# Optimization experiments

Hardware: AMD Instinct MI355X
Metric: run time of the kernel (lower is better)

## Reference

```python
import jax, jax.numpy as jnp
import numpy as np

N = 768       # num nodes
E = 12288     # num edges (avg degree 16)
D_IN = 6
H = 256       # hidden_dim
TEMPERATURE = 1.0


def gcn_conv(x, W, b, src, dst, n):
    """PyG GCNConv: add self-loops, symmetric deg^-1/2 normalization, then xW aggregation + bias."""
    h = x @ W  # [n, H]
    loop = jnp.arange(n, dtype=src.dtype)
    s = jnp.concatenate([src, loop])
    d = jnp.concatenate([dst, loop])
    deg = jax.ops.segment_sum(jnp.ones(s.shape, dtype=h.dtype), d, num_segments=n)
    dinv = jnp.where(deg > 0, jax.lax.rsqrt(deg), 0.0)
    norm = dinv[s] * dinv[d]  # [E+n]
    out = jax.ops.segment_sum(h[s] * norm[:, None], d, num_segments=n)
    return out + b


def setup_inputs() -> dict:
    key = jax.random.key(0)
    ks = jax.random.split(key, 10)
    sc = lambda fan: np.float32(1.0 / np.sqrt(fan))
    x = jax.random.normal(ks[0], (N, D_IN), jnp.float32)
    edge_index = jax.random.randint(ks[1], (2, E), 0, N, dtype=jnp.int32)
    Wc1 = jax.random.normal(ks[2], (D_IN, H), jnp.float32) * sc(D_IN)
    bc1 = jnp.zeros((H,), jnp.float32)
    Wc2 = jax.random.normal(ks[3], (H, H), jnp.float32) * sc(H)
    bc2 = jnp.zeros((H,), jnp.float32)
    We1 = jax.random.normal(ks[4], (2 * H, H), jnp.float32) * sc(2 * H)
    be1 = jax.random.normal(ks[5], (H,), jnp.float32) * sc(2 * H)
    We2 = jax.random.normal(ks[6], (H, 1), jnp.float32) * sc(H)
    be2 = jax.random.normal(ks[7], (1,), jnp.float32) * sc(H)
    return {"x": x, "edge_index": edge_index, "Wc1": Wc1, "bc1": bc1,
            "Wc2": Wc2, "bc2": bc2, "We1": We1, "be1": be1, "We2": We2, "be2": be2}


def reference(x, edge_index, Wc1, bc1, Wc2, bc2, We1, be1, We2, be2):
    src, dst = edge_index[0], edge_index[1]
    h = jax.nn.elu(gcn_conv(x, Wc1, bc1, src, dst, N))
    h = gcn_conv(h, Wc2, bc2, src, dst, N)  # [N, H]
    # edge scorer: Linear(cat([x_i, x_j])) == x_i @ We1[:H] + x_j @ We1[H:] + be1
    ai = h @ We1[:H]   # [N, H], contribution of x_i (row node)
    aj = h @ We1[H:]   # [N, H], contribution of x_j (col node)
    pair = jax.nn.relu(ai[:, None, :] + aj[None, :, :] + be1)  # [N, N, H]
    logits = jnp.einsum('ijh,h->ij', pair, We2[:, 0]) + be2[0]  # [N, N]
    logits = logits / TEMPERATURE
    logits = jnp.where(jnp.eye(N, dtype=bool), -jnp.inf, logits)
    return jax.nn.softmax(logits, axis=-1)
```

## Files before the change

### kernel.cpp

```cpp
#include <hip/hip_runtime.h>
#include <math.h>

#define N_NODES 768
#define N_EDGES 12288
#define D_INF 6
#define H 256
#define CAP 128
#define SA 260

__global__ __launch_bounds__(768) void k_zero(int* __restrict__ cnt) {
    cnt[threadIdx.x] = 0;
}

__global__ void k_scatter(const int* __restrict__ src, const int* __restrict__ dst,
                          int* __restrict__ cnt, int* __restrict__ slots) {
    int e = blockIdx.x * blockDim.x + threadIdx.x;
    if (e >= N_EDGES) return;
    int d = dst[e];
    int p = atomicAdd(&cnt[d], 1);
    if (p < CAP) slots[d * CAP + p] = src[e];
}

__global__ __launch_bounds__(256) void k_layer1(
    const float* __restrict__ x, const float* __restrict__ Wc1,
    const float* __restrict__ bc1, const int* __restrict__ cnt,
    const int* __restrict__ slots, float* __restrict__ h1) {
    __shared__ int   s_s[CAP];
    __shared__ float s_w[CAP];
    __shared__ float s6[D_INF];
    const int v = blockIdx.x, t = threadIdx.x;
    const int c = cnt[v];
    const int cc = min(c, CAP);
    const float dv = rsqrtf((float)(c + 1));

    if (t < D_INF) s6[t] = dv * dv * x[v * D_INF + t];
    for (int i = t; i < cc; i += 256) {
        int s = slots[v * CAP + i];
        s_s[i] = s;
        s_w[i] = rsqrtf((float)(cnt[s] + 1)) * dv;
    }
    __syncthreads();
    for (int i = t; i < D_INF * cc; i += 256) {
        int n = i / D_INF, k = i - n * D_INF;
        atomicAdd(&s6[k], s_w[n] * x[s_s[n] * D_INF + k]);
    }
    __syncthreads();
    float acc = bc1[t];
    #pragma unroll
    for (int k = 0; k < D_INF; ++k) acc = fmaf(s6[k], Wc1[k * H + t], acc);
    h1[v * H + t] = (acc > 0.f) ? acc : expm1f(acc);
}

__global__ __launch_bounds__(256) void k_agg(
    const float* __restrict__ h1, const int* __restrict__ cnt,
    const int* __restrict__ slots, float* __restrict__ agg2) {
    __shared__ int   s_s[CAP];
    __shared__ float s_w[CAP];
    const int v = blockIdx.x, t = threadIdx.x;
    const int c = cnt[v];
    const int cc = min(c, CAP);
    const float dv = rsqrtf((float)(c + 1));

    for (int i = t; i < cc; i += 256) {
        int s = slots[v * CAP + i];
        s_s[i] = s;
        s_w[i] = rsqrtf((float)(cnt[s] + 1)) * dv;
    }
    __syncthreads();
    float acc = dv * dv * h1[v * H + t];
    #pragma unroll 4
    for (int n = 0; n < cc; ++n)
        acc = fmaf(s_w[n], h1[s_s[n] * H + t], acc);
    agg2[v * H + t] = acc;
}

__global__ __launch_bounds__(256) void k_h2(
    const float* __restrict__ agg2, const float* __restrict__ Wc2,
    const float* __restrict__ bc2, float* __restrict__ h2) {
    __shared__ __align__(16) float s_a[48 * SA];
    __shared__ __align__(16) float s_wT[16 * SA];
    const int t = threadIdx.x, b = blockIdx.x;
    const int rg = b >> 4, cp = b & 15;
    const int j0 = rg * 48, c0 = cp * 16;
    const int c = t & 15, ro = t >> 4;

    for (int i = t; i < 48 * 64; i += 256) {
        int r = i >> 6, q = i & 63;
        float4 v = *(const float4*)(agg2 + (size_t)(j0 + r) * H + q * 4);
        *(float4*)&s_a[r * SA + q * 4] = v;
    }
    {
        int kk = t >> 4, cc = t & 15;
        #pragma unroll
        for (int it = 0; it < 16; ++it) {
            int k = kk + it * 16;
            s_wT[cc * SA + k] = Wc2[(size_t)k * H + c0 + cc];
        }
    }
    __syncthreads();

    float a0 = 0.f, a1 = 0.f, a2 = 0.f;
    #pragma unroll 8
    for (int kg = 0; kg < 64; ++kg) {
        float4 w  = *(const float4*)&s_wT[c * SA + kg * 4];
        float4 v0 = *(const float4*)&s_a[(ro)      * SA + kg * 4];
        float4 v1 = *(const float4*)&s_a[(ro + 16) * SA + kg * 4];
        float4 v2 = *(const float4*)&s_a[(ro + 32) * SA + kg * 4];
        a0 = fmaf(v0.x, w.x, a0); a0 = fmaf(v0.y, w.y, a0);
        a0 = fmaf(v0.z, w.z, a0); a0 = fmaf(v0.w, w.w, a0);
        a1 = fmaf(v1.x, w.x, a1); a1 = fmaf(v1.y, w.y, a1);
        a1 = fmaf(v1.z, w.z, a1); a1 = fmaf(v1.w, w.w, a1);
        a2 = fmaf(v2.x, w.x, a2); a2 = fmaf(v2.y, w.y, a2);
        a2 = fmaf(v2.z, w.z, a2); a2 = fmaf(v2.w, w.w, a2);
    }
    float bb = bc2[c0 + c];
    h2[(size_t)(j0 + ro)      * H + c0 + c] = a0 + bb;
    h2[(size_t)(j0 + ro + 16) * H + c0 + c] = a1 + bb;
    h2[(size_t)(j0 + ro + 32) * H + c0 + c] = a2 + bb;
}

__global__ __launch_bounds__(256) void k_ae(
    const float* __restrict__ h2, const float* __restrict__ We1,
    const float* __restrict__ be1, float* __restrict__ aib,
    float* __restrict__ ajcT) {
    __shared__ __align__(16) float s_h[32 * SA];
    __shared__ __align__(16) float s_waT[16 * SA];
    __shared__ __align__(16) float s_wbT[16 * SA];
    const int t = threadIdx.x, b = blockIdx.x;
    const int rg = b >> 4, cp = b & 15;
    const int j0 = rg * 32, c0 = cp * 16;
    const int c = t & 15, ro = t >> 4;

    for (int i = t; i < 32 * 64; i += 256) {
        int r = i >> 6, q = i & 63;
        float4 v = *(const float4*)(h2 + (size_t)(j0 + r) * H + q * 4);
        *(float4*)&s_h[r * SA + q * 4] = v;
    }
    {
        int kk = t >> 4, cc = t & 15;
        #pragma unroll
        for (int it = 0; it < 16; ++it) {
            int k = kk + it * 16;
            s_waT[cc * SA + k] = We1[(size_t)k * H + c0 + cc];
            s_wbT[cc * SA + k] = We1[(size_t)(H + k) * H + c0 + cc];
        }
    }
    __syncthreads();

    float pa0 = 0.f, pa1 = 0.f, pb0 = 0.f, pb1 = 0.f;
    #pragma unroll 8
    for (int kg = 0; kg < 64; ++kg) {
        float4 wa = *(const float4*)&s_waT[c * SA + kg * 4];
        float4 wb = *(const float4*)&s_wbT[c * SA + kg * 4];
        float4 v0 = *(const float4*)&s_h[(ro)      * SA + kg * 4];
        float4 v1 = *(const float4*)&s_h[(ro + 16) * SA + kg * 4];
        pa0 = fmaf(v0.x, wa.x, pa0); pa0 = fmaf(v0.y, wa.y, pa0);
        pa0 = fmaf(v0.z, wa.z, pa0); pa0 = fmaf(v0.w, wa.w, pa0);
        pa1 = fmaf(v1.x, wa.x, pa1); pa1 = fmaf(v1.y, wa.y, pa1);
        pa1 = fmaf(v1.z, wa.z, pa1); pa1 = fmaf(v1.w, wa.w, pa1);
        pb0 = fmaf(v0.x, wb.x, pb0); pb0 = fmaf(v0.y, wb.y, pb0);
        pb0 = fmaf(v0.z, wb.z, pb0); pb0 = fmaf(v0.w, wb.w, pb0);
        pb1 = fmaf(v1.x, wb.x, pb1); pb1 = fmaf(v1.y, wb.y, pb1);
        pb1 = fmaf(v1.z, wb.z, pb1); pb1 = fmaf(v1.w, wb.w, pb1);
    }
    aib[(size_t)(j0 + ro)      * H + c0 + c] = pa0;
    aib[(size_t)(j0 + ro + 16) * H + c0 + c] = pa1;
    float be = be1[c0 + c];
    ajcT[(size_t)(c0 + c) * N_NODES + j0 + ro]      = pb0 + be;
    ajcT[(size_t)(c0 + c) * N_NODES + j0 + ro + 16] = pb1 + be;
}

__global__ __launch_bounds__(1024) void k_pair(
    const float* __restrict__ aib, const float* __restrict__ ajcT,
    const float* __restrict__ We2, float* __restrict__ out) {
    __shared__ float s_ai[3 * H];
    __shared__ float s_w2[H];
    __shared__ float s_acc[3 * 9 * 256];
    __shared__ float red[3 * 256];
    const int t = threadIdx.x, b = blockIdx.x;
    const int tc = t & 255, th = t >> 8;
    const int i0 = b * 3;

    if (th == 0) s_w2[tc] = We2[tc];
    else s_ai[(th - 1) * H + tc] = aib[(i0 + th - 1) * H + tc];
    __syncthreads();

    float acc[3][3];
    #pragma unroll
    for (int i = 0; i < 3; ++i)
        #pragma unroll
        for (int jj = 0; jj < 3; ++jj) acc[i][jj] = 0.f;

    const int hb = th * 64;
    #pragma unroll 8
    for (int hh = 0; hh < 64; ++hh) {
        int h = hb + hh;
        float wv = s_w2[h];
        float a0v = s_ai[h], a1v = s_ai[256 + h], a2v = s_ai[512 + h];
        const float* col = ajcT + (size_t)h * N_NODES;
        float b0 = col[tc], b1 = col[tc + 256], b2 = col[tc + 512];
        acc[0][0] = fmaf(fmaxf(a0v + b0, 0.f), wv, acc[0][0]);
        acc[0][1] = fmaf(fmaxf(a0v + b1, 0.f), wv, acc[0][1]);
        acc[0][2] = fmaf(fmaxf(a0v + b2, 0.f), wv, acc[0][2]);
        acc[1][0] = fmaf(fmaxf(a1v + b0, 0.f), wv, acc[1][0]);
        acc[1][1] = fmaf(fmaxf(a1v + b1, 0.f), wv, acc[1][1]);
        acc[1][2] = fmaf(fmaxf(a1v + b2, 0.f), wv, acc[1][2]);
        acc[2][0] = fmaf(fmaxf(a2v + b0, 0.f), wv, acc[2][0]);
        acc[2][1] = fmaf(fmaxf(a2v + b1, 0.f), wv, acc[2][1]);
        acc[2][2] = fmaf(fmaxf(a2v + b2, 0.f), wv, acc[2][2]);
    }

    if (th > 0) {
        #pragma unroll
        for (int i = 0; i < 3; ++i)
            #pragma unroll
            for (int jj = 0; jj < 3; ++jj)
                s_acc[((th - 1) * 9 + i * 3 + jj) * 256 + tc] = acc[i][jj];
    }
    __syncthreads();
    if (th == 0) {
        #pragma unroll
        for (int qq = 0; qq < 3; ++qq)
            #pragma unroll
            for (int i = 0; i < 3; ++i)
                #pragma unroll
                for (int jj = 0; jj < 3; ++jj)
                    acc[i][jj] += s_acc[(qq * 9 + i * 3 + jj) * 256 + tc];
        #pragma unroll
        for (int i = 0; i < 3; ++i)
            #pragma unroll
            for (int jj = 0; jj < 3; ++jj)
                if (tc + jj * 256 == i0 + i) acc[i][jj] = -INFINITY;
        #pragma unroll
        for (int i = 0; i < 3; ++i)
            red[i * 256 + tc] = fmaxf(fmaxf(acc[i][0], acc[i][1]), acc[i][2]);
    }
    __syncthreads();
    for (int s = 128; s > 0; s >>= 1) {
        if (t < s) {
            red[t] = fmaxf(red[t], red[t + s]);
            red[256 + t] = fmaxf(red[256 + t], red[256 + t + s]);
            red[512 + t] = fmaxf(red[512 + t], red[512 + t + s]);
        }
        __syncthreads();
    }
    float mx0 = red[0], mx1 = red[256], mx2 = red[512];
    __syncthreads();

    float e[3][3];
    if (th == 0) {
        float s0 = 0.f, s1 = 0.f, s2 = 0.f;
        #pragma unroll
        for (int jj = 0; jj < 3; ++jj) {
            e[0][jj] = __expf(acc[0][jj] - mx0); s0 += e[0][jj];
            e[1][jj] = __expf(acc[1][jj] - mx1); s1 += e[1][jj];
            e[2][jj] = __expf(acc[2][jj] - mx2); s2 += e[2][jj];
        }
        red[tc] = s0; red[256 + tc] = s1; red[512 + tc] = s2;
    }
    __syncthreads();
    for (int s = 128; s > 0; s >>= 1) {
        if (t < s) {
            red[t] += red[t + s];
            red[256 + t] += red[256 + t + s];
            red[512 + t] += red[512 + t + s];
        }
        __syncthreads();
    }
    if (th == 0) {
        float r0 = 1.0f / red[0], r1 = 1.0f / red[256], r2 = 1.0f / red[512];
        #pragma unroll
        for (int jj = 0; jj < 3; ++jj) {
            out[(size_t)(i0 + 0) * N_NODES + tc + jj * 256] = e[0][jj] * r0;
            out[(size_t)(i0 + 1) * N_NODES + tc + jj * 256] = e[1][jj] * r1;
            out[(size_t)(i0 + 2) * N_NODES + tc + jj * 256] = e[2][jj] * r2;
        }
    }
}

extern "C" void kernel_launch(void* const* d_in, const int* in_sizes, int n_in,
                              void* d_out, int out_size, void* d_ws, size_t ws_size,
                              hipStream_t stream) {
    const float* x   = (const float*)d_in[0];
    const int*   ei  = (const int*)d_in[1];
    const float* Wc1 = (const float*)d_in[2];
    const float* bc1 = (const float*)d_in[3];
    const float* Wc2 = (const float*)d_in[4];
    const float* bc2 = (const float*)d_in[5];
    const float* We1 = (const float*)d_in[6];
    const float* be1 = (const float*)d_in[7];
    const float* We2 = (const float*)d_in[8];
    float* out = (float*)d_out;

    char* ws = (char*)d_ws;
    int*   cnt   = (int*)(ws + 0);
    int*   slots = (int*)(ws + 4096);
    float* h1    = (float*)(ws + 397312);
    float* agg2  = (float*)(ws + 1183744);
    float* ajcT  = (float*)(ws + 1970176);
    float* h2    = h1;
    float* aib   = agg2;

    const int* srcA = ei;
    const int* dstA = ei + N_EDGES;

    k_zero<<<1, 768, 0, stream>>>(cnt);
    k_scatter<<<N_EDGES / 256, 256, 0, stream>>>(srcA, dstA, cnt, slots);
    k_layer1<<<N_NODES, 256, 0, stream>>>(x, Wc1, bc1, cnt, slots, h1);
    k_agg<<<N_NODES, 256, 0, stream>>>(h1, cnt, slots, agg2);
    k_h2<<<256, 256, 0, stream>>>(agg2, Wc2, bc2, h2);
    k_ae<<<384, 256, 0, stream>>>(h2, We1, be1, aib, ajcT);
    k_pair<<<N_NODES / 3, 1024, 0, stream>>>(aib, ajcT, We2, out);
}
```

Measured before the change: 58.62 us.

## Fuse graph front-end, precompose Wc2·We1, split pair scoring from softmax

Replaces the zero/scatter/layer1 kernels with one front kernel in which each block redundantly counts degrees over all edges in shared memory and builds its own nodes' neighbor lists. The same launch also precomputes Wc2·[We1a|We1b] and the folded bias, so one GEMM replaces the h2 and edge-embedding GEMMs. The pair-scoring kernel is re-tiled to 12 rows by a quarter of the hidden dim, writing partial logits to workspace, and a separate softmax kernel sums the partials. This cuts launch count and GEMM work, but every front block rescans all edges and the partial logits add extra global traffic.

```diff
diff --git a/kernel.cpp b/kernel.cpp
--- a/kernel.cpp
+++ b/kernel.cpp
@@ -5,50 +5,120 @@
 #define N_EDGES 12288
 #define D_INF 6
 #define H 256
+#define H2 512
 #define CAP 128
+#define LC 256
 #define SA 260
 
-__global__ __launch_bounds__(768) void k_zero(int* __restrict__ cnt) {
-    cnt[threadIdx.x] = 0;
-}
-
-__global__ void k_scatter(const int* __restrict__ src, const int* __restrict__ dst,
-                          int* __restrict__ cnt, int* __restrict__ slots) {
-    int e = blockIdx.x * blockDim.x + threadIdx.x;
-    if (e >= N_EDGES) return;
-    int d = dst[e];
-    int p = atomicAdd(&cnt[d], 1);
-    if (p < CAP) slots[d * CAP + p] = src[e];
-}
-
-__global__ __launch_bounds__(256) void k_layer1(
-    const float* __restrict__ x, const float* __restrict__ Wc1,
-    const float* __restrict__ bc1, const int* __restrict__ cnt,
-    const int* __restrict__ slots, float* __restrict__ h1) {
-    __shared__ int   s_s[CAP];
-    __shared__ float s_w[CAP];
-    __shared__ float s6[D_INF];
-    const int v = blockIdx.x, t = threadIdx.x;
-    const int c = cnt[v];
-    const int cc = min(c, CAP);
-    const float dv = rsqrtf((float)(c + 1));
-
-    if (t < D_INF) s6[t] = dv * dv * x[v * D_INF + t];
-    for (int i = t; i < cc; i += 256) {
-        int s = slots[v * CAP + i];
-        s_s[i] = s;
-        s_w[i] = rsqrtf((float)(cnt[s] + 1)) * dv;
-    }
-    __syncthreads();
-    for (int i = t; i < D_INF * cc; i += 256) {
-        int n = i / D_INF, k = i - n * D_INF;
-        atomicAdd(&s6[k], s_w[n] * x[s_s[n] * D_INF + k]);
-    }
-    __syncthreads();
-    float acc = bc1[t];
-    #pragma unroll
-    for (int k = 0; k < D_INF; ++k) acc = fmaf(s6[k], Wc1[k * H + t], acc);
-    h1[v * H + t] = (acc > 0.f) ? acc : expm1f(acc);
+__global__ __launch_bounds__(256) void k_front(
+    const float* __restrict__ x, const int* __restrict__ ei,
+    const float* __restrict__ Wc1, const float* __restrict__ bc1,
+    const float* __restrict__ Wc2, const float* __restrict__ bc2,
+    const float* __restrict__ We1, const float* __restrict__ be1,
+    int* __restrict__ cnt_g, int* __restrict__ slots,
+    float* __restrict__ h1, float* __restrict__ Wcombo, float* __restrict__ bias_c)
+{
+    const int t = threadIdx.x;
+    if (blockIdx.x < 256) {
+        __shared__ int s_cnt[N_NODES];
+        __shared__ int s_list[LC];
+        __shared__ int s_nm;
+        __shared__ int s_pos[3];
+        __shared__ float s_agg[3][D_INF];
+        const int b = blockIdx.x, v0 = b * 3;
+        const int* src = ei;
+        const int* dst = ei + N_EDGES;
+        for (int v = t; v < N_NODES; v += 256) s_cnt[v] = 0;
+        if (t == 0) s_nm = 0;
+        if (t < 3) s_pos[t] = 0;
+        if (t < 3 * D_INF) ((float*)s_agg)[t] = 0.f;
+        __syncthreads();
+        for (int e = t; e < N_EDGES; e += 256) {
+            int d = dst[e];
+            atomicAdd(&s_cnt[d], 1);
+            unsigned li = (unsigned)(d - v0);
+            if (li < 3u) {
+                int s = src[e];
+                int p = atomicAdd(&s_nm, 1);
+                if (p < LC) s_list[p] = (s << 2) | (int)li;
+            }
+        }
+        __syncthreads();
+        const int nm = min(s_nm, LC);
+        if (t < 3) cnt_g[v0 + t] = s_cnt[v0 + t];
+        for (int m = t; m < nm; m += 256) {
+            int pk = s_list[m];
+            int s = pk >> 2, li = pk & 3;
+            int p = atomicAdd(&s_pos[li], 1);
+            if (p < CAP) slots[(v0 + li) * CAP + p] = s;
+            float w = rsqrtf((float)(s_cnt[s] + 1)) * rsqrtf((float)(s_cnt[v0 + li] + 1));
+            #pragma unroll
+            for (int k = 0; k < D_INF; ++k)
+                atomicAdd(&s_agg[li][k], w * x[s * D_INF + k]);
+        }
+        if (t < 3) {
+            int v = v0 + t;
+            float dv2 = 1.0f / (float)(s_cnt[v] + 1);
+            #pragma unroll
+            for (int k = 0; k < D_INF; ++k)
+                atomicAdd(&s_agg[t][k], dv2 * x[v * D_INF + k]);
+        }
+        __syncthreads();
+        #pragma unroll
+        for (int r = 0; r < 3; ++r) {
+            float acc = bc1[t];
+            #pragma unroll
+            for (int k = 0; k < D_INF; ++k)
+                acc = fmaf(s_agg[r][k], Wc1[k * H + t], acc);
+            h1[(v0 + r) * H + t] = (acc > 0.f) ? acc : expm1f(acc);
+        }
+    } else {
+        __shared__ __align__(16) float s_a[32 * SA];
+        __shared__ __align__(16) float s_bT[16 * SA];
+        __shared__ float s_bc2[H];
+        const int idx = blockIdx.x - 256;
+        const int rg = idx >> 5, cp = idx & 31;
+        const int r0 = rg * 32, c0 = cp * 16;
+        const int c = t & 15, ro = t >> 4;
+        for (int i = t; i < 32 * 64; i += 256) {
+            int r = i >> 6, q = i & 63;
+            float4 v = *(const float4*)(Wc2 + (size_t)(r0 + r) * H + q * 4);
+            *(float4*)&s_a[r * SA + q * 4] = v;
+        }
+        {
+            int kk = t >> 4, cc = t & 15;
+            int cg = c0 + cc;
+            const float* Wsrc = (cg < H) ? (We1 + cg)
+                                         : (We1 + (size_t)H * H + (cg - H));
+            #pragma unroll
+            for (int it = 0; it < 16; ++it) {
+                int k = kk + it * 16;
+                s_bT[cc * SA + k] = Wsrc[(size_t)k * H];
+            }
+        }
+        s_bc2[t] = bc2[t];
+        __syncthreads();
+        float a0 = 0.f, a1 = 0.f;
+        #pragma unroll 8
+        for (int kg = 0; kg < 64; ++kg) {
+            float4 w  = *(const float4*)&s_bT[c * SA + kg * 4];
+            float4 v0 = *(const float4*)&s_a[(ro)      * SA + kg * 4];
+            float4 v1 = *(const float4*)&s_a[(ro + 16) * SA + kg * 4];
+            a0 = fmaf(v0.x, w.x, a0); a0 = fmaf(v0.y, w.y, a0);
+            a0 = fmaf(v0.z, w.z, a0); a0 = fmaf(v0.w, w.w, a0);
+            a1 = fmaf(v1.x, w.x, a1); a1 = fmaf(v1.y, w.y, a1);
+            a1 = fmaf(v1.z, w.z, a1); a1 = fmaf(v1.w, w.w, a1);
+        }
+        Wcombo[(size_t)(r0 + ro)      * H2 + c0 + c] = a0;
+        Wcombo[(size_t)(r0 + ro + 16) * H2 + c0 + c] = a1;
+        if (rg == 0 && t < 16) {
+            int cg = c0 + t;
+            float bias = (cg >= H) ? be1[cg - H] : 0.f;
+            for (int k = 0; k < H; ++k)
+                bias = fmaf(s_bc2[k], s_bT[t * SA + k], bias);
+            bias_c[cg] = bias;
+        }
+    }
 }
 
 __global__ __launch_bounds__(256) void k_agg(
@@ -60,7 +130,6 @@
     const int c = cnt[v];
     const int cc = min(c, CAP);
     const float dv = rsqrtf((float)(c + 1));
-
     for (int i = t; i < cc; i += 256) {
         int s = slots[v * CAP + i];
         s_s[i] = s;
@@ -74,208 +143,134 @@
     agg2[v * H + t] = acc;
 }
 
-__global__ __launch_bounds__(256) void k_h2(
-    const float* __restrict__ agg2, const float* __restrict__ Wc2,
-    const float* __restrict__ bc2, float* __restrict__ h2) {
-    __shared__ __align__(16) float s_a[48 * SA];
+__global__ __launch_bounds__(256) void k_ae2(
+    const float* __restrict__ agg2, const float* __restrict__ Wcombo,
+    const float* __restrict__ bias_c, float* __restrict__ aib,
+    float* __restrict__ ajcT) {
+    __shared__ __align__(16) float s_h[32 * SA];
     __shared__ __align__(16) float s_wT[16 * SA];
     const int t = threadIdx.x, b = blockIdx.x;
-    const int rg = b >> 4, cp = b & 15;
-    const int j0 = rg * 48, c0 = cp * 16;
+    const int rg = b >> 5, cp = b & 31;
+    const int j0 = rg * 32, c0 = cp * 16;
     const int c = t & 15, ro = t >> 4;
 
-    for (int i = t; i < 48 * 64; i += 256) {
+    for (int i = t; i < 32 * 64; i += 256) {
         int r = i >> 6, q = i & 63;
         float4 v = *(const float4*)(agg2 + (size_t)(j0 + r) * H + q * 4);
-        *(float4*)&s_a[r * SA + q * 4] = v;
+        *(float4*)&s_h[r * SA + q * 4] = v;
     }
     {
         int kk = t >> 4, cc = t & 15;
         #pragma unroll
         for (int it = 0; it < 16; ++it) {
             int k = kk + it * 16;
-            s_wT[cc * SA + k] = Wc2[(size_t)k * H + c0 + cc];
-        }
-    }
-    __syncthreads();
-
-    float a0 = 0.f, a1 = 0.f, a2 = 0.f;
+            s_wT[cc * SA + k] = Wcombo[(size_t)k * H2 + c0 + cc];
+        }
+    }
+    __syncthreads();
+
+    float pa0 = 0.f, pa1 = 0.f;
     #pragma unroll 8
     for (int kg = 0; kg < 64; ++kg) {
         float4 w  = *(const float4*)&s_wT[c * SA + kg * 4];
-        float4 v0 = *(const float4*)&s_a[(ro)      * SA + kg * 4];
-        float4 v1 = *(const float4*)&s_a[(ro + 16) * SA + kg * 4];
-        float4 v2 = *(const float4*)&s_a[(ro + 32) * SA + kg * 4];
-        a0 = fmaf(v0.x, w.x, a0); a0 = fmaf(v0.y, w.y, a0);
-        a0 = fmaf(v0.z, w.z, a0); a0 = fmaf(v0.w, w.w, a0);
-        a1 = fmaf(v1.x, w.x, a1); a1 = fmaf(v1.y, w.y, a1);
-        a1 = fmaf(v1.z, w.z, a1); a1 = fmaf(v1.w, w.w, a1);
-        a2 = fmaf(v2.x, w.x, a2); a2 = fmaf(v2.y, w.y, a2);
-        a2 = fmaf(v2.z, w.z, a2); a2 = fmaf(v2.w, w.w, a2);
-    }
-    float bb = bc2[c0 + c];
-    h2[(size_t)(j0 + ro)      * H + c0 + c] = a0 + bb;
-    h2[(size_t)(j0 + ro + 16) * H + c0 + c] = a1 + bb;
-    h2[(size_t)(j0 + ro + 32) * H + c0 + c] = a2 + bb;
-}
-
-__global__ __launch_bounds__(256) void k_ae(
-    const float* __restrict__ h2, const float* __restrict__ We1,
-    const float* __restrict__ be1, float* __restrict__ aib,
-    float* __restrict__ ajcT) {
-    __shared__ __align__(16) float s_h[32 * SA];
-    __shared__ __align__(16) float s_waT[16 * SA];
-    __shared__ __align__(16) float s_wbT[16 * SA];
-    const int t = threadIdx.x, b = blockIdx.x;
-    const int rg = b >> 4, cp = b & 15;
-    const int j0 = rg * 32, c0 = cp * 16;
-    const int c = t & 15, ro = t >> 4;
-
-    for (int i = t; i < 32 * 64; i += 256) {
-        int r = i >> 6, q = i & 63;
-        float4 v = *(const float4*)(h2 + (size_t)(j0 + r) * H + q * 4);
-        *(float4*)&s_h[r * SA + q * 4] = v;
-    }
-    {
-        int kk = t >> 4, cc = t & 15;
-        #pragma unroll
-        for (int it = 0; it < 16; ++it) {
-            int k = kk + it * 16;
-            s_waT[cc * SA + k] = We1[(size_t)k * H + c0 + cc];
-            s_wbT[cc * SA + k] = We1[(size_t)(H + k) * H + c0 + cc];
-        }
-    }
-    __syncthreads();
-
-    float pa0 = 0.f, pa1 = 0.f, pb0 = 0.f, pb1 = 0.f;
-    #pragma unroll 8
-    for (int kg = 0; kg < 64; ++kg) {
-        float4 wa = *(const float4*)&s_waT[c * SA + kg * 4];
-        float4 wb = *(const float4*)&s_wbT[c * SA + kg * 4];
         float4 v0 = *(const float4*)&s_h[(ro)      * SA + kg * 4];
         float4 v1 = *(const float4*)&s_h[(ro + 16) * SA + kg * 4];
-        pa0 = fmaf(v0.x, wa.x, pa0); pa0 = fmaf(v0.y, wa.y, pa0);
-        pa0 = fmaf(v0.z, wa.z, pa0); pa0 = fmaf(v0.w, wa.w, pa0);
-        pa1 = fmaf(v1.x, wa.x, pa1); pa1 = fmaf(v1.y, wa.y, pa1);
-        pa1 = fmaf(v1.z, wa.z, pa1); pa1 = fmaf(v1.w, wa.w, pa1);
-        pb0 = fmaf(v0.x, wb.x, pb0); pb0 = fmaf(v0.y, wb.y, pb0);
-        pb0 = fmaf(v0.z, wb.z, pb0); pb0 = fmaf(v0.w, wb.w, pb0);
-        pb1 = fmaf(v1.x, wb.x, pb1); pb1 = fmaf(v1.y, wb.y, pb1);
-        pb1 = fmaf(v1.z, wb.z, pb1); pb1 = fmaf(v1.w, wb.w, pb1);
-    }
-    aib[(size_t)(j0 + ro)      * H + c0 + c] = pa0;
-    aib[(size_t)(j0 + ro + 16) * H + c0 + c] = pa1;
-    float be = be1[c0 + c];
-    ajcT[(size_t)(c0 + c) * N_NODES + j0 + ro]      = pb0 + be;
-    ajcT[(size_t)(c0 + c) * N_NODES + j0 + ro + 16] = pb1 + be;
-}
-
-__global__ __launch_bounds__(1024) void k_pair(
+        pa0 = fmaf(v0.x, w.x, pa0); pa0 = fmaf(v0.y, w.y, pa0);
+        pa0 = fmaf(v0.z, w.z, pa0); pa0 = fmaf(v0.w, w.w, pa0);
+        pa1 = fmaf(v1.x, w.x, pa1); pa1 = fmaf(v1.y, w.y, pa1);
+        pa1 = fmaf(v1.z, w.z, pa1); pa1 = fmaf(v1.w, w.w, pa1);
+    }
+    int cg = c0 + c;
+    float bb = bias_c[cg];
+    if (cg < H) {
+        aib[(size_t)(j0 + ro)      * H + cg] = pa0 + bb;
+        aib[(size_t)(j0 + ro + 16) * H + cg] = pa1 + bb;
+    } else {
+        ajcT[(size_t)(cg - H) * N_NODES + j0 + ro]      = pa0 + bb;
+        ajcT[(size_t)(cg - H) * N_NODES + j0 + ro + 16] = pa1 + bb;
+    }
+}
+
+__global__ __launch_bounds__(512) void k_pairA(
     const float* __restrict__ aib, const float* __restrict__ ajcT,
-    const float* __restrict__ We2, float* __restrict__ out) {
-    __shared__ float s_ai[3 * H];
+    const float* __restrict__ We2, float* __restrict__ logits_p) {
+    __shared__ float s_ai[12 * H];
     __shared__ float s_w2[H];
-    __shared__ float s_acc[3 * 9 * 256];
-    __shared__ float red[3 * 256];
     const int t = threadIdx.x, b = blockIdx.x;
     const int tc = t & 255, th = t >> 8;
-    const int i0 = b * 3;
-
-    if (th == 0) s_w2[tc] = We2[tc];
-    else s_ai[(th - 1) * H + tc] = aib[(i0 + th - 1) * H + tc];
-    __syncthreads();
-
-    float acc[3][3];
+    const int rg = b >> 2, hp = b & 3;
+    const int i0 = rg * 12, h0 = hp * 64;
+
+    for (int i = t; i < 12 * H; i += 512) {
+        int r = i >> 8, col = i & 255;
+        s_ai[r * H + col] = aib[(size_t)(i0 + r) * H + col];
+    }
+    if (t < H) s_w2[t] = We2[t];
+    __syncthreads();
+
+    const int r0 = th * 6;
+    float acc[6][3];
     #pragma unroll
-    for (int i = 0; i < 3; ++i)
-        #pragma unroll
-        for (int jj = 0; jj < 3; ++jj) acc[i][jj] = 0.f;
-
-    const int hb = th * 64;
-    #pragma unroll 8
+    for (int r = 0; r < 6; ++r)
+        #pragma unroll
+        for (int jj = 0; jj < 3; ++jj) acc[r][jj] = 0.f;
+
+    #pragma unroll 4
     for (int hh = 0; hh < 64; ++hh) {
-        int h = hb + hh;
+        int h = h0 + hh;
         float wv = s_w2[h];
-        float a0v = s_ai[h], a1v = s_ai[256 + h], a2v = s_ai[512 + h];
         const float* col = ajcT + (size_t)h * N_NODES;
         float b0 = col[tc], b1 = col[tc + 256], b2 = col[tc + 512];
-        acc[0][0] = fmaf(fmaxf(a0v + b0, 0.f), wv, acc[0][0]);
-        acc[0][1] = fmaf(fmaxf(a0v + b1, 0.f), wv, acc[0][1]);
-        acc[0][2] = fmaf(fmaxf(a0v + b2, 0.f), wv, acc[0][2]);
-        acc[1][0] = fmaf(fmaxf(a1v + b0, 0.f), wv, acc[1][0]);
-        acc[1][1] = fmaf(fmaxf(a1v + b1, 0.f), wv, acc[1][1]);
-        acc[1][2] = fmaf(fmaxf(a1v + b2, 0.f), wv, acc[1][2]);
-        acc[2][0] = fmaf(fmaxf(a2v + b0, 0.f), wv, acc[2][0]);
-        acc[2][1] = fmaf(fmaxf(a2v + b1, 0.f), wv, acc[2][1]);
-        acc[2][2] = fmaf(fmaxf(a2v + b2, 0.f), wv, acc[2][2]);
-    }
-
-    if (th > 0) {
-        #pragma unroll
-        for (int i = 0; i < 3; ++i)
-            #pragma unroll
-            for (int jj = 0; jj < 3; ++jj)
-                s_acc[((th - 1) * 9 + i * 3 + jj) * 256 + tc] = acc[i][jj];
-    }
-    __syncthreads();
-    if (th == 0) {
-        #pragma unroll
-        for (int qq = 0; qq < 3; ++qq)
-            #pragma unroll
-            for (int i = 0; i < 3; ++i)
-                #pragma unroll
-                for (int jj = 0; jj < 3; ++jj)
-                    acc[i][jj] += s_acc[(qq * 9 + i * 3 + jj) * 256 + tc];
-        #pragma unroll
-        for (int i = 0; i < 3; ++i)
-            #pragma unroll
-            for (int jj = 0; jj < 3; ++jj)
-                if (tc + jj * 256 == i0 + i) acc[i][jj] = -INFINITY;
-        #pragma unroll
-        for (int i = 0; i < 3; ++i)
-            red[i * 256 + tc] = fmaxf(fmaxf(acc[i][0], acc[i][1]), acc[i][2]);
-    }
+        #pragma unroll
+        for (int r = 0; r < 6; ++r) {
+            float av = s_ai[(r0 + r) * H + h];
+            acc[r][0] = fmaf(fmaxf(av + b0, 0.f), wv, acc[r][0]);
+            acc[r][1] = fmaf(fmaxf(av + b1, 0.f), wv, acc[r][1]);
+            acc[r][2] = fmaf(fmaxf(av + b2, 0.f), wv, acc[r][2]);
+        }
+    }
+    #pragma unroll
+    for (int r = 0; r < 6; ++r) {
+        float* row = logits_p + ((size_t)hp * N_NODES + i0 + r0 + r) * N_NODES;
+        #pragma unroll
+        for (int jj = 0; jj < 3; ++jj)
+            row[tc + jj * 256] = acc[r][jj];
+    }
+}
+
+__global__ __launch_bounds__(256) void k_soft(
+    const float* __restrict__ logits_p, float* __restrict__ out) {
+    __shared__ float red[256];
+    const int i = blockIdx.x, t = threadIdx.x;
+    float l[3];
+    #pragma unroll
+    for (int jj = 0; jj < 3; ++jj) {
+        int j = t + jj * 256;
+        float s = 0.f;
+        #pragma unroll
+        for (int hp = 0; hp < 4; ++hp)
+            s += logits_p[((size_t)hp * N_NODES + i) * N_NODES + j];
+        l[jj] = (j == i) ? -INFINITY : s;
+    }
+    red[t] = fmaxf(fmaxf(l[0], l[1]), l[2]);
     __syncthreads();
     for (int s = 128; s > 0; s >>= 1) {
-        if (t < s) {
-            red[t] = fmaxf(red[t], red[t + s]);
-            red[256 + t] = fmaxf(red[256 + t], red[256 + t + s]);
-            red[512 + t] = fmaxf(red[512 + t], red[512 + t + s]);
-        }
-        __syncthreads();
-    }
-    float mx0 = red[0], mx1 = red[256], mx2 = red[512];
-    __syncthreads();
-
-    float e[3][3];
-    if (th == 0) {
-        float s0 = 0.f, s1 = 0.f, s2 = 0.f;
-        #pragma unroll
-        for (int jj = 0; jj < 3; ++jj) {
-            e[0][jj] = __expf(acc[0][jj] - mx0); s0 += e[0][jj];
-            e[1][jj] = __expf(acc[1][jj] - mx1); s1 += e[1][jj];
-            e[2][jj] = __expf(acc[2][jj] - mx2); s2 += e[2][jj];
-        }
-        red[tc] = s0; red[256 + tc] = s1; red[512 + tc] = s2;
-    }
+        if (t < s) red[t] = fmaxf(red[t], red[t + s]);
+        __syncthreads();
+    }
+    float mx = red[0];
+    __syncthreads();
+    float e0 = __expf(l[0] - mx), e1 = __expf(l[1] - mx), e2 = __expf(l[2] - mx);
+    red[t] = e0 + e1 + e2;
     __syncthreads();
     for (int s = 128; s > 0; s >>= 1) {
-        if (t < s) {
-            red[t] += red[t + s];
-            red[256 + t] += red[256 + t + s];
-            red[512 + t] += red[512 + t + s];
-        }
-        __syncthreads();
-    }
-    if (th == 0) {
-        float r0 = 1.0f / red[0], r1 = 1.0f / red[256], r2 = 1.0f / red[512];
-        #pragma unroll
-        for (int jj = 0; jj < 3; ++jj) {
-            out[(size_t)(i0 + 0) * N_NODES + tc + jj * 256] = e[0][jj] * r0;
-            out[(size_t)(i0 + 1) * N_NODES + tc + jj * 256] = e[1][jj] * r1;
-            out[(size_t)(i0 + 2) * N_NODES + tc + jj * 256] = e[2][jj] * r2;
-        }
-    }
+        if (t < s) red[t] += red[t + s];
+        __syncthreads();
+    }
+    float inv = 1.0f / red[0];
+    out[(size_t)i * N_NODES + t]       = e0 * inv;
+    out[(size_t)i * N_NODES + t + 256] = e1 * inv;
+    out[(size_t)i * N_NODES + t + 512] = e2 * inv;
 }
 
 extern "C" void kernel_launch(void* const* d_in, const int* in_sizes, int n_in,
@@ -293,22 +288,20 @@
     float* out = (float*)d_out;
 
     char* ws = (char*)d_ws;
-    int*   cnt   = (int*)(ws + 0);
-    int*   slots = (int*)(ws + 4096);
-    float* h1    = (float*)(ws + 397312);
-    float* agg2  = (float*)(ws + 1183744);
-    float* ajcT  = (float*)(ws + 1970176);
-    float* h2    = h1;
-    float* aib   = agg2;
-
-    const int* srcA = ei;
-    const int* dstA = ei + N_EDGES;
-
-    k_zero<<<1, 768, 0, stream>>>(cnt);
-    k_scatter<<<N_EDGES / 256, 256, 0, stream>>>(srcA, dstA, cnt, slots);
-    k_layer1<<<N_NODES, 256, 0, stream>>>(x, Wc1, bc1, cnt, slots, h1);
+    int*   cnt      = (int*)(ws + 0);
+    int*   slots    = (int*)(ws + 4096);
+    float* h1       = (float*)(ws + 397312);
+    float* agg2     = (float*)(ws + 1183744);
+    float* aib      = (float*)(ws + 1970176);
+    float* ajcT     = (float*)(ws + 2756608);
+    float* Wcombo   = (float*)(ws + 3543040);
+    float* bias_c   = (float*)(ws + 4067328);
+    float* logits_p = (float*)(ws + 4069376);
+
+    k_front<<<512, 256, 0, stream>>>(x, ei, Wc1, bc1, Wc2, bc2, We1, be1,
+                                     cnt, slots, h1, Wcombo, bias_c);
     k_agg<<<N_NODES, 256, 0, stream>>>(h1, cnt, slots, agg2);
-    k_h2<<<256, 256, 0, stream>>>(agg2, Wc2, bc2, h2);
-    k_ae<<<384, 256, 0, stream>>>(h2, We1, be1, aib, ajcT);
-    k_pair<<<N_NODES / 3, 1024, 0, stream>>>(aib, ajcT, We2, out);
-}
+    k_ae2<<<768, 256, 0, stream>>>(agg2, Wcombo, bias_c, aib, ajcT);
+    k_pairA<<<256, 512, 0, stream>>>(aib, ajcT, We2, logits_p);
+    k_soft<<<N_NODES, 256, 0, stream>>>(logits_p, out);
+}
```

New measurement: 57.30 us. -2.2%, faster.
